# Optimization experiments

Measured on AMD Instinct MI355X. Metric: run time of the kernel, lower is better.

Reference implementation:

```python
import jax, jax.numpy as jnp
import numpy as np

D_MODEL = 1024
HEADS = 16
D_K = D_MODEL // HEADS
D_FF = 4096
EPS = 1e-6


def setup_inputs() -> dict:
    key = jax.random.key(0)
    ks = jax.random.split(key, 16)
    s = 1.0 / np.sqrt(D_MODEL)
    inp = {
        'x': jax.random.normal(ks[0], (4, 2048, D_MODEL), dtype=jnp.float32),
        'Wq': jax.random.normal(ks[1], (D_MODEL, D_MODEL), dtype=jnp.float32) * s,
        'bq': jnp.zeros((D_MODEL,), jnp.float32),
        'Wk': jax.random.normal(ks[2], (D_MODEL, D_MODEL), dtype=jnp.float32) * s,
        'bk': jnp.zeros((D_MODEL,), jnp.float32),
        'Wv': jax.random.normal(ks[3], (D_MODEL, D_MODEL), dtype=jnp.float32) * s,
        'bv': jnp.zeros((D_MODEL,), jnp.float32),
        'Wo': jax.random.normal(ks[4], (D_MODEL, D_MODEL), dtype=jnp.float32) * s,
        'bo': jnp.zeros((D_MODEL,), jnp.float32),
        'alpha1': jnp.ones((D_MODEL,), jnp.float32),
        'bias1': jnp.zeros((D_MODEL,), jnp.float32),
        'alpha2': jnp.ones((D_MODEL,), jnp.float32),
        'bias2': jnp.zeros((D_MODEL,), jnp.float32),
        'W1': jax.random.normal(ks[5], (D_MODEL, D_FF), dtype=jnp.float32) * s,
        'b1': jnp.zeros((D_FF,), jnp.float32),
        'W2': jax.random.normal(ks[6], (D_FF, D_MODEL), dtype=jnp.float32) * (1.0 / np.sqrt(D_FF)),
        'b2': jnp.zeros((D_MODEL,), jnp.float32),
    }
    return inp


def _residual_norm(x, residual, alpha, bias):
    # x = x + residual; norm with mean and UNBIASED std (torch x.std default),
    # eps added to std (not variance), affine alpha/bias. Dropout = identity (eval).
    s = x + residual
    mean = jnp.mean(s, axis=-1, keepdims=True)
    std = jnp.std(s, axis=-1, keepdims=True, ddof=1)
    return alpha * (s - mean) / (std + EPS) + bias


def _forward(x, Wq, bq, Wk, bk, Wv, bv, Wo, bo, alpha1, bias1, alpha2, bias2, W1, b1, W2, b2):
    B, S, D = x.shape
    # QKV projections and head split: (B, H, S, d_k)
    def split_heads(t):
        return t.reshape(B, S, HEADS, D_K).transpose(0, 2, 1, 3)
    Q = split_heads(x @ Wq + bq)
    K = split_heads(x @ Wk + bk)
    V = split_heads(x @ Wv + bv)
    # scaled dot-product attention (no mask, no dropout in eval)
    scores = jnp.einsum('bhqd,bhkd->bhqk', Q, K) / np.sqrt(D_K)
    weights = jax.nn.softmax(scores, axis=-1)
    attn = jnp.einsum('bhqk,bhkd->bhqd', weights, V)
    concat = attn.transpose(0, 2, 1, 3).reshape(B, S, D)
    attn_out = concat @ Wo + bo
    # post-norm residual 1
    norm1 = _residual_norm(attn_out, x, alpha1, bias1)
    # FFN (dropout = identity in eval)
    ff = jax.nn.relu(norm1 @ W1 + b1) @ W2 + b2
    # post-norm residual 2
    return _residual_norm(ff, norm1, alpha2, bias2)


def reference(x, Wq, bq, Wk, bk, Wv, bv, Wo, bo, alpha1, bias1, alpha2, bias2, W1, b1, W2, b2):
    return _forward(x, Wq, bq, Wk, bk, Wv, bv, Wo, bo, alpha1, bias1, alpha2, bias2, W1, b1, W2, b2)
```

## Files before the change

### kernel.cpp

```cpp
#include <hip/hip_runtime.h>
#include <hip/hip_bf16.h>
#include <stdint.h>

typedef __attribute__((ext_vector_type(8))) short bv8;
typedef __attribute__((ext_vector_type(4))) short sv4;
typedef __attribute__((ext_vector_type(4))) float f4;
typedef __attribute__((ext_vector_type(4))) unsigned uv4;

#define LDS_AS __attribute__((address_space(3)))
#define GLB_AS __attribute__((address_space(1)))

#if __has_builtin(__builtin_amdgcn_exp2f)
#define EXP2F(x) __builtin_amdgcn_exp2f(x)
#else
#define EXP2F(x) exp2f(x)
#endif

#define GBAR __builtin_amdgcn_s_barrier()

__device__ __forceinline__ void gload16(const void* g, void* l) {
  __builtin_amdgcn_global_load_lds((GLB_AS void*)(g), (LDS_AS void*)(l), 16, 0, 0);
}

__device__ __forceinline__ short f2bs(float x) {
  return __builtin_bit_cast(short, __float2bfloat16(x));
}
__device__ __forceinline__ float bs2f(short s) {
  unsigned u = ((unsigned)(unsigned short)s) << 16;
  return __builtin_bit_cast(float, u);
}
__device__ __forceinline__ unsigned cvtpk(float lo, float hi) {
  unsigned r;
  asm("v_cvt_pk_bf16_f32 %0, %1, %2" : "=v"(r) : "v"(lo), "v"(hi));
  return r;
}

__global__ __launch_bounds__(256) void k_prep(const float* __restrict__ x, short* __restrict__ xb,
                                              const float* __restrict__ Wq, short* __restrict__ Wqt,
                                              const float* __restrict__ Wk, short* __restrict__ Wkt,
                                              const float* __restrict__ Wv, short* __restrict__ Wvt,
                                              const float* __restrict__ Wo, short* __restrict__ Wot,
                                              const float* __restrict__ W1, short* __restrict__ W1t,
                                              const float* __restrict__ W2, short* __restrict__ W2t) {
  const int bid = blockIdx.x;
  if (bid < 8192) {
    const int i = (bid * 256 + threadIdx.x) * 4;
    const float4 v = *(const float4*)(x + i);
    sv4 o; o[0] = f2bs(v.x); o[1] = f2bs(v.y); o[2] = f2bs(v.z); o[3] = f2bs(v.w);
    *(sv4*)(xb + i) = o;
    return;
  }
  const float* W; short* Wt; int K, N, l;
  if (bid < 12288) {
    l = (bid - 8192) & 1023; K = 1024; N = 1024;
    const int sel = (bid - 8192) >> 10;
    W  = sel == 0 ? Wq  : sel == 1 ? Wk  : sel == 2 ? Wv  : Wo;
    Wt = sel == 0 ? Wqt : sel == 1 ? Wkt : sel == 2 ? Wvt : Wot;
  } else if (bid < 16384) {
    l = bid - 12288; K = 1024; N = 4096; W = W1; Wt = W1t;
  } else {
    l = bid - 16384; K = 4096; N = 1024; W = W2; Wt = W2t;
  }
  const int nb = N >> 5;
  const int n0 = (l % nb) * 32, k0 = (l / nb) * 32;
  __shared__ float tile[32][33];
  const int tx = threadIdx.x & 31, ty = threadIdx.x >> 5;
#pragma unroll
  for (int i = 0; i < 32; i += 8)
    tile[ty + i][tx] = W[(size_t)(k0 + ty + i) * N + n0 + tx];
  __syncthreads();
#pragma unroll
  for (int i = 0; i < 32; i += 8)
    Wt[(size_t)(n0 + ty + i) * K + k0 + tx] = f2bs(tile[tx][ty + i]);
}

template<int EPI, int MIH>
__global__ __launch_bounds__(512) void k_gemm8p(
    const short* __restrict__ A, const short* __restrict__ Bt,
    const float* __restrict__ bias, const float* __restrict__ bias2, const float* __restrict__ bias3,
    short* __restrict__ C, short* __restrict__ D2, short* __restrict__ D3,
    int M, int N, int K, int nbx) {
  constexpr int BM = MIH * 64;
  constexpr int HOFF = (MIH == 4) ? 16384 : 4096;
  __shared__ __align__(16) short SA[2][BM * 64];
  __shared__ __align__(16) short SB[2][256 * 64];

  const int t = threadIdx.x;
  const int lane = t & 63, w = t >> 6;
  const int wr = w >> 2, wc = w & 3;
  const int lr = lane & 15, lg = lane >> 4;
  const int cpx = gridDim.x >> 3;
  const int bid = blockIdx.x;
  const int wid = (bid & 7) * cpx + (bid >> 3);
  const int by = wid / nbx, bx = wid % nbx;
  const int m0 = by * BM, n0 = bx * 256;
  const int nt = K >> 6;
  const int swz = ((t >> 3) & 7) << 4;
  const int rbyte0 = (lg * 16) ^ ((lr & 7) << 4);
  const int rbyte1 = (64 + lg * 16) ^ ((lr & 7) << 4);

  auto ST_A = [&](int k0, int half, int buf) {
#pragma unroll
    for (int i = 0; i < 2; ++i) {
      const int L = t * 16 + i * 8192;
      const int cbs = (L & 127) ^ swz;
      const int grow = (MIH == 4) ? (m0 + i * 128 + half * 64 + (t >> 3))
                                  : (m0 + i * 64 + (t >> 3));
      gload16(A + (size_t)grow * K + k0 + (cbs >> 1),
              (char*)SA[buf] + (MIH == 4 ? half * 16384 : 0) + L);
    }
  };
  auto ST_B = [&](int k0, int half, int buf) {
#pragma unroll
    for (int i = 0; i < 2; ++i) {
      const int L = t * 16 + i * 8192;
      const int rr = (t >> 3) + i * 64;
      const int cbs = (L & 127) ^ swz;
      const int grow = n0 + (rr >> 5) * 64 + half * 32 + (rr & 31);
      gload16(Bt + (size_t)grow * K + k0 + (cbs >> 1),
              (char*)SB[buf] + half * 16384 + L);
    }
  };

  f4 acc[2 * MIH][4] = {};
  bv8 af[MIH][2], bflo[2][2], bfhi[2][2];

  auto LDA = [&](int buf, int half) {
    const char* base = (const char*)SA[buf] + half * HOFF + wr * 8192;
#pragma unroll
    for (int m = 0; m < MIH; ++m) {
      af[m][0] = *(const bv8*)(base + (m * 16 + lr) * 128 + rbyte0);
      af[m][1] = *(const bv8*)(base + (m * 16 + lr) * 128 + rbyte1);
    }
  };
  auto LDB = [&](int buf, int half, bv8 (&bf)[2][2]) {
    const char* base = (const char*)SB[buf] + half * 16384 + wc * 4096;
#pragma unroll
    for (int n = 0; n < 2; ++n) {
      bf[n][0] = *(const bv8*)(base + (n * 16 + lr) * 128 + rbyte0);
      bf[n][1] = *(const bv8*)(base + (n * 16 + lr) * 128 + rbyte1);
    }
  };
  auto MM = [&](bv8 (&bf)[2][2], int mB, int nB) {
    __builtin_amdgcn_s_setprio(1);
#pragma unroll
    for (int kk = 0; kk < 2; ++kk)
#pragma unroll
      for (int m = 0; m < MIH; ++m)
#pragma unroll
        for (int n = 0; n < 2; ++n)
          acc[mB + m][nB + n] = __builtin_amdgcn_mfma_f32_16x16x32_bf16(
              af[m][kk], bf[n][kk], acc[mB + m][nB + n], 0, 0, 0);
    __builtin_amdgcn_s_setprio(0);
  };

  ST_A(0, 0, 0); if (MIH == 4) ST_A(0, 1, 0);
  ST_B(0, 0, 0); ST_B(0, 1, 0);
  ST_A(64, 0, 1);
  ST_B(64, 1, 1);
  if (MIH == 4) { ST_A(64, 1, 1); asm volatile("s_waitcnt vmcnt(6)" ::: "memory"); }
  else          { asm volatile("s_waitcnt vmcnt(4)" ::: "memory"); }
  GBAR;

  const int nIter = nt >> 1;
  for (int it = 0; it < nIter; ++it) {
    const int k1 = (2 * it + 1) << 6;
    const int k2 = (2 * it + 2) << 6, k3 = (2 * it + 3) << 6;
    const bool h2 = (2 * it + 2) < nt, h3 = (2 * it + 3) < nt;

    LDA(0, 0); LDB(0, 0, bflo);
    ST_B(k1, 0, 1);
    GBAR; MM(bflo, 0, 0); GBAR;
    LDB(0, 1, bfhi);
    if (h2 && MIH == 4) ST_A(k2, 0, 0);
    GBAR; MM(bfhi, 0, 2); GBAR;
    LDA(0, 1);
    if (h2) ST_B(k2, 1, 0);
    GBAR; MM(bfhi, MIH, 2); GBAR;
    if (h2) ST_A(k2, (MIH == 4) ? 1 : 0, 0);
    if (h2) {
      if (MIH == 4) asm volatile("s_waitcnt vmcnt(6)" ::: "memory");
      else          asm volatile("s_waitcnt vmcnt(4)" ::: "memory");
    } else {
      asm volatile("s_waitcnt vmcnt(0)" ::: "memory");
    }
    GBAR; MM(bflo, MIH, 0); GBAR;

    LDA(1, 0); LDB(1, 0, bflo);
    if (h2) ST_B(k2, 0, 0);
    GBAR; MM(bflo, 0, 0); GBAR;
    LDB(1, 1, bfhi);
    if (h3 && MIH == 4) ST_A(k3, 0, 1);
    GBAR; MM(bfhi, 0, 2); GBAR;
    LDA(1, 1);
    if (h3) ST_B(k3, 1, 1);
    GBAR; MM(bfhi, MIH, 2); GBAR;
    if (h3) ST_A(k3, (MIH == 4) ? 1 : 0, 1);
    if (h3) {
      if (MIH == 4) asm volatile("s_waitcnt vmcnt(6)" ::: "memory");
      else          asm volatile("s_waitcnt vmcnt(4)" ::: "memory");
    } else {
      asm volatile("s_waitcnt vmcnt(0)" ::: "memory");
    }
    GBAR; MM(bflo, MIH, 0); GBAR;
  }

#pragma unroll
  for (int ni = 0; ni < 4; ++ni) {
    const int c = n0 + wc * 64 + ni * 16 + lr;
    float bvs;
    int sel = 0, h = 0, d = 0;
    if (EPI == 2) {
      sel = c >> 10; const int cc = c & 1023;
      bvs = (sel == 0 ? bias : sel == 1 ? bias2 : bias3)[cc];
      h = cc >> 6; d = cc & 63;
    } else {
      bvs = bias[c];
    }
#pragma unroll
    for (int mi = 0; mi < 2 * MIH; ++mi) {
#pragma unroll
      for (int j = 0; j < 4; ++j) {
        const int r = m0 + wr * (MIH * 32) + mi * 16 + lg * 4 + j;
        float v = acc[mi][ni][j] + bvs;
        if (EPI == 1) v = fmaxf(v, 0.f);
        if (EPI == 2) {
          const int bb = r >> 11, s = r & 2047;
          if (sel == 0)      C [((size_t)(bb * 16 + h) * 2048 + s) * 64 + d] = f2bs(v);
          else if (sel == 1) D2[((size_t)(bb * 16 + h) * 2048 + s) * 64 + d] = f2bs(v);
          else               D3[((size_t)(bb * 16 + h) * 64 + d) * 2048 + s] = f2bs(v);
        } else {
          C[(size_t)r * N + c] = f2bs(v);
        }
      }
    }
  }
}

__global__ __launch_bounds__(256) void k_attn(const short* __restrict__ Qg, const short* __restrict__ Kg,
                                              const short* __restrict__ Vtg, short* __restrict__ Oc) {
  __shared__ __align__(16) short Ks[2][128 * 64];

  const int t = threadIdx.x, lane = t & 63, w = t >> 6;
  const int lr = lane & 15, lg = lane >> 4;
  const int bid = blockIdx.x;
  const int wid = (bid & 7) * 128 + (bid >> 3);
  const int q0 = (wid & 15) * 128;
  const int bh = wid >> 4;
  const int b = bh >> 4, h = bh & 15;
  const short* Qp = Qg + (size_t)bh * 2048 * 64;
  const short* Kp = Kg + (size_t)bh * 2048 * 64;
  const short* Vp = Vtg + (size_t)bh * 64 * 2048;

  bv8 qf[2][2];
#pragma unroll
  for (int mi = 0; mi < 2; ++mi)
#pragma unroll
    for (int kk = 0; kk < 2; ++kk)
      qf[mi][kk] = *(const bv8*)(Qp + (size_t)(q0 + w * 32 + mi * 16 + lr) * 64 + kk * 32 + lg * 8);

  f4 Oa[2][4] = {};
  float lsum[2] = {0.f, 0.f};
  const float SC = 0.125f * 1.44269504089f;
  const bool hi = lg >= 2;
  const bool xx = (lg == 1) || (lg == 2);

  auto QKSM = [&](const char* Kb, int hf, bv8 (&pf)[2][2]) {
    f4 Sa[2][4] = {};
#pragma unroll
    for (int kk = 0; kk < 2; ++kk) {
      bv8 kf[4];
#pragma unroll
      for (int nl = 0; nl < 4; ++nl) {
        const int row = (hf * 4 + nl) * 16 + lr;
        const int cb = kk * 64 + lg * 16;
        kf[nl] = *(const bv8*)(Kb + row * 128 + (cb ^ ((row & 7) << 4)));
      }
      __builtin_amdgcn_s_setprio(1);
#pragma unroll
      for (int mi = 0; mi < 2; ++mi)
#pragma unroll
        for (int nl = 0; nl < 4; ++nl)
          Sa[mi][nl] = __builtin_amdgcn_mfma_f32_16x16x32_bf16(kf[nl], qf[mi][kk], Sa[mi][nl], 0, 0, 0);
      __builtin_amdgcn_s_setprio(0);
    }
#pragma unroll
    for (int mi = 0; mi < 2; ++mi) {
      float rs = 0.f;
#pragma unroll
      for (int nl = 0; nl < 4; ++nl)
#pragma unroll
        for (int j = 0; j < 4; ++j) {
          const float p = EXP2F(Sa[mi][nl][j] * SC);
          Sa[mi][nl][j] = p;
          rs += p;
        }
      lsum[mi] += rs;
    }
#pragma unroll
    for (int k2 = 0; k2 < 2; ++k2)
#pragma unroll
      for (int mi = 0; mi < 2; ++mi) {
        const unsigned W0 = cvtpk(Sa[mi][2 * k2][0], Sa[mi][2 * k2][1]);
        const unsigned W1 = cvtpk(Sa[mi][2 * k2][2], Sa[mi][2 * k2][3]);
        const unsigned W2 = cvtpk(Sa[mi][2 * k2 + 1][0], Sa[mi][2 * k2 + 1][1]);
        const unsigned W3 = cvtpk(Sa[mi][2 * k2 + 1][2], Sa[mi][2 * k2 + 1][3]);
        const unsigned w0 = hi ? W2 : W0, w1 = hi ? W3 : W1;
        const unsigned s0 = __shfl_xor(hi ? W0 : W2, 32);
        const unsigned s1 = __shfl_xor(hi ? W1 : W3, 32);
        const unsigned t0 = __shfl_xor(xx ? w0 : s0, 16);
        const unsigned t1 = __shfl_xor(xx ? w1 : s1, 16);
        uv4 u;
        u[0] = (lg == 0) ? w0 : (lg == 2) ? s0 : t0;
        u[1] = (lg == 0) ? w1 : (lg == 2) ? s1 : t1;
        u[2] = (lg == 3) ? w0 : (lg == 1) ? s0 : t0;
        u[3] = (lg == 3) ? w1 : (lg == 1) ? s1 : t1;
        pf[k2][mi] = __builtin_bit_cast(bv8, u);
      }
  };
  auto LOADV = [&](int kt, int hf, bv8 (&vf)[2][4]) {
#pragma unroll
    for (int k2 = 0; k2 < 2; ++k2)
#pragma unroll
      for (int nO = 0; nO < 4; ++nO)
        vf[k2][nO] = *(const bv8*)(Vp + (size_t)(nO * 16 + lr) * 2048 + kt + hf * 64 + k2 * 32 + lg * 8);
  };
  auto PV = [&](bv8 (&vf)[2][4], bv8 (&pf)[2][2]) {
    __builtin_amdgcn_s_setprio(1);
#pragma unroll
    for (int k2 = 0; k2 < 2; ++k2)
#pragma unroll
      for (int mi = 0; mi < 2; ++mi)
#pragma unroll
        for (int nO = 0; nO < 4; ++nO)
          Oa[mi][nO] = __builtin_amdgcn_mfma_f32_16x16x32_bf16(vf[k2][nO], pf[k2][mi], Oa[mi][nO], 0, 0, 0);
    __builtin_amdgcn_s_setprio(0);
  };

#pragma unroll
  for (int i = 0; i < 4; ++i) {
    const int L = t * 16 + i * 4096;
    const int row = L >> 7;
    const int cbs = (L & 127) ^ ((row & 7) << 4);
    gload16(Kp + (size_t)row * 64 + (cbs >> 1), (char*)Ks[0] + L);
  }
  __syncthreads();

  int cur = 0;
  for (int kt = 0; kt < 2048; kt += 128) {
    if (kt + 128 < 2048) {
#pragma unroll
      for (int i = 0; i < 4; ++i) {
        const int L = t * 16 + i * 4096;
        const int row = L >> 7;
        const int cbs = (L & 127) ^ ((row & 7) << 4);
        gload16(Kp + (size_t)(kt + 128 + row) * 64 + (cbs >> 1), (char*)Ks[cur ^ 1] + L);
      }
    }
    const char* Kb = (const char*)Ks[cur];

    bv8 vfA[2][4], vfB[2][4], pfA[2][2], pfB[2][2];
    LOADV(kt, 0, vfA);
    QKSM(Kb, 0, pfA);
    LOADV(kt, 1, vfB);
    PV(vfA, pfA);
    QKSM(Kb, 1, pfB);
    PV(vfB, pfB);

    __syncthreads();
    cur ^= 1;
  }

#pragma unroll
  for (int mi = 0; mi < 2; ++mi) {
    lsum[mi] += __shfl_xor(lsum[mi], 16);
    lsum[mi] += __shfl_xor(lsum[mi], 32);
  }

#pragma unroll
  for (int mi = 0; mi < 2; ++mi) {
    const float inv = 1.f / lsum[mi];
    const int q = q0 + w * 32 + mi * 16 + lr;
#pragma unroll
    for (int nO = 0; nO < 4; ++nO) {
      sv4 o;
#pragma unroll
      for (int j = 0; j < 4; ++j) o[j] = f2bs(Oa[mi][nO][j] * inv);
      const int c = h * 64 + nO * 16 + lg * 4;
      *(sv4*)(Oc + ((size_t)b * 2048 + q) * 1024 + c) = o;
    }
  }
}

template<int MODE>
__global__ __launch_bounds__(256) void k_resnorm(const short* __restrict__ a, const void* __restrict__ res,
                                                 const float* __restrict__ alpha, const float* __restrict__ beta,
                                                 void* __restrict__ out) {
  const int row = blockIdx.x;
  const int t = threadIdx.x;
  const int lane = t & 63, w = t >> 6;
  const size_t base = (size_t)row * 1024;

  const sv4 av = *(const sv4*)(a + base + t * 4);
  float v[4];
  if (MODE == 0) {
    const float4 rv = *(const float4*)((const float*)res + base + t * 4);
    v[0] = bs2f(av[0]) + rv.x; v[1] = bs2f(av[1]) + rv.y;
    v[2] = bs2f(av[2]) + rv.z; v[3] = bs2f(av[3]) + rv.w;
  } else {
    const sv4 rv = *(const sv4*)((const short*)res + base + t * 4);
#pragma unroll
    for (int i = 0; i < 4; ++i) v[i] = bs2f(av[i]) + bs2f(rv[i]);
  }
  float s = v[0] + v[1] + v[2] + v[3];
  float sq = v[0] * v[0] + v[1] * v[1] + v[2] * v[2] + v[3] * v[3];
#pragma unroll
  for (int m = 1; m < 64; m <<= 1) { s += __shfl_xor(s, m); sq += __shfl_xor(sq, m); }
  __shared__ float red[8];
  if (lane == 0) { red[w] = s; red[w + 4] = sq; }
  __syncthreads();
  s = red[0] + red[1] + red[2] + red[3];
  sq = red[4] + red[5] + red[6] + red[7];
  const float mean = s * (1.f / 1024.f);
  const float var = (sq - 1024.f * mean * mean) * (1.f / 1023.f);
  const float inv = 1.f / (sqrtf(fmaxf(var, 0.f)) + 1e-6f);
  const float4 al = *(const float4*)(alpha + t * 4);
  const float4 be = *(const float4*)(beta + t * 4);
  float y[4];
  y[0] = al.x * (v[0] - mean) * inv + be.x;
  y[1] = al.y * (v[1] - mean) * inv + be.y;
  y[2] = al.z * (v[2] - mean) * inv + be.z;
  y[3] = al.w * (v[3] - mean) * inv + be.w;
  if (MODE == 0) {
    sv4 o; o[0] = f2bs(y[0]); o[1] = f2bs(y[1]); o[2] = f2bs(y[2]); o[3] = f2bs(y[3]);
    *(sv4*)((short*)out + base + t * 4) = o;
  } else {
    *(float4*)((float*)out + base + t * 4) = make_float4(y[0], y[1], y[2], y[3]);
  }
}

extern "C" void kernel_launch(void* const* d_in, const int* in_sizes, int n_in,
                              void* d_out, int out_size, void* d_ws, size_t ws_size,
                              hipStream_t stream) {
  const float* x   = (const float*)d_in[0];
  const float* Wq  = (const float*)d_in[1];
  const float* bq  = (const float*)d_in[2];
  const float* Wk  = (const float*)d_in[3];
  const float* bk  = (const float*)d_in[4];
  const float* Wv  = (const float*)d_in[5];
  const float* bv  = (const float*)d_in[6];
  const float* Wo  = (const float*)d_in[7];
  const float* bo  = (const float*)d_in[8];
  const float* al1 = (const float*)d_in[9];
  const float* bi1 = (const float*)d_in[10];
  const float* al2 = (const float*)d_in[11];
  const float* bi2 = (const float*)d_in[12];
  const float* W1  = (const float*)d_in[13];
  const float* b1  = (const float*)d_in[14];
  const float* W2  = (const float*)d_in[15];
  const float* b2  = (const float*)d_in[16];

  if (ws_size < (size_t)136 * 1024 * 1024) return;

  char* ws = (char*)d_ws;
  short* xb  = (short*)(ws);
  short* Qb  = (short*)(ws + (16ll << 20));
  short* Kb  = (short*)(ws + (32ll << 20));
  short* Vtb = (short*)(ws + (48ll << 20));
  short* Hb  = (short*)(ws);
  short* Wqt = (short*)(ws + (64ll << 20));
  short* Wkt = (short*)(ws + (66ll << 20));
  short* Wvt = (short*)(ws + (68ll << 20));
  short* Wot = (short*)(ws + (70ll << 20));
  short* W1t = (short*)(ws + (72ll << 20));
  short* W2t = (short*)(ws + (80ll << 20));
  short* Cc  = (short*)(ws + (88ll << 20));
  short* AOb = (short*)(ws + (104ll << 20));
  short* N1b = (short*)(ws + (120ll << 20));
  short* FFb = (short*)(ws + (104ll << 20));

  k_prep<<<20480, 256, 0, stream>>>(x, xb, Wq, Wqt, Wk, Wkt, Wv, Wvt, Wo, Wot, W1, W1t, W2, W2t);

  k_gemm8p<2, 2><<<768, 512, 0, stream>>>(xb, Wqt, bq, bk, bv, Qb, Kb, Vtb, 8192, 3072, 1024, 12);

  k_attn<<<1024, 256, 0, stream>>>(Qb, Kb, Vtb, Cc);

  k_gemm8p<0, 2><<<256, 512, 0, stream>>>(Cc, Wot, bo, nullptr, nullptr, AOb, nullptr, nullptr,
                                          8192, 1024, 1024, 4);
  k_resnorm<0><<<8192, 256, 0, stream>>>(AOb, x, al1, bi1, N1b);

  k_gemm8p<1, 4><<<512, 512, 0, stream>>>(N1b, W1t, b1, nullptr, nullptr, Hb, nullptr, nullptr,
                                          8192, 4096, 1024, 16);
  k_gemm8p<0, 2><<<256, 512, 0, stream>>>(Hb, W2t, b2, nullptr, nullptr, FFb, nullptr, nullptr,
                                          8192, 1024, 4096, 4);
  k_resnorm<1><<<8192, 256, 0, stream>>>(FFb, N1b, al2, bi2, (float*)d_out);
}
```

Before: 449.7 us.

## Stage transposed V epilogue through LDS and prefetch V fragments ahead

The QKV GEMM epilogue for the V section now writes bias-added bf16 results into a shared LDS buffer in transposed layout, then emits coalesced 16-byte row stores to the V^T output. The previous path did scattered 2-byte strided stores. The attention kernel also software-pipelines the V fragment loads by issuing the first half-tile load for the next iteration early. The LDS transpose path only writes output when MIH==2, so other tile configurations would silently skip V output. The prefetch adds register pressure.

```diff
diff --git a/kernel.cpp b/kernel.cpp
--- a/kernel.cpp
+++ b/kernel.cpp
@@ -82,8 +82,8 @@
     int M, int N, int K, int nbx) {
   constexpr int BM = MIH * 64;
   constexpr int HOFF = (MIH == 4) ? 16384 : 4096;
-  __shared__ __align__(16) short SA[2][BM * 64];
-  __shared__ __align__(16) short SB[2][256 * 64];
+  constexpr int SBOFF = 2 * BM * 128;
+  __shared__ __align__(16) char LDSBUF[SBOFF + 65536];
 
   const int t = threadIdx.x;
   const int lane = t & 63, w = t >> 6;
@@ -99,6 +99,9 @@
   const int rbyte0 = (lg * 16) ^ ((lr & 7) << 4);
   const int rbyte1 = (64 + lg * 16) ^ ((lr & 7) << 4);
 
+  auto SAb = [&](int buf) -> char* { return LDSBUF + buf * (BM * 128); };
+  auto SBb = [&](int buf) -> char* { return LDSBUF + SBOFF + buf * 32768; };
+
   auto ST_A = [&](int k0, int half, int buf) {
 #pragma unroll
     for (int i = 0; i < 2; ++i) {
@@ -107,7 +110,7 @@
       const int grow = (MIH == 4) ? (m0 + i * 128 + half * 64 + (t >> 3))
                                   : (m0 + i * 64 + (t >> 3));
       gload16(A + (size_t)grow * K + k0 + (cbs >> 1),
-              (char*)SA[buf] + (MIH == 4 ? half * 16384 : 0) + L);
+              SAb(buf) + (MIH == 4 ? half * 16384 : 0) + L);
     }
   };
   auto ST_B = [&](int k0, int half, int buf) {
@@ -118,7 +121,7 @@
       const int cbs = (L & 127) ^ swz;
       const int grow = n0 + (rr >> 5) * 64 + half * 32 + (rr & 31);
       gload16(Bt + (size_t)grow * K + k0 + (cbs >> 1),
-              (char*)SB[buf] + half * 16384 + L);
+              SBb(buf) + half * 16384 + L);
     }
   };
 
@@ -126,7 +129,7 @@
   bv8 af[MIH][2], bflo[2][2], bfhi[2][2];
 
   auto LDA = [&](int buf, int half) {
-    const char* base = (const char*)SA[buf] + half * HOFF + wr * 8192;
+    const char* base = SAb(buf) + half * HOFF + wr * 8192;
 #pragma unroll
     for (int m = 0; m < MIH; ++m) {
       af[m][0] = *(const bv8*)(base + (m * 16 + lr) * 128 + rbyte0);
@@ -134,7 +137,7 @@
     }
   };
   auto LDB = [&](int buf, int half, bv8 (&bf)[2][2]) {
-    const char* base = (const char*)SB[buf] + half * 16384 + wc * 4096;
+    const char* base = SBb(buf) + half * 16384 + wc * 4096;
 #pragma unroll
     for (int n = 0; n < 2; ++n) {
       bf[n][0] = *(const bv8*)(base + (n * 16 + lr) * 128 + rbyte0);
@@ -205,6 +208,36 @@
     GBAR; MM(bflo, MIH, 0); GBAR;
   }
 
+  if (EPI == 2 && (n0 >> 10) == 2) {
+    short* TR = (short*)LDSBUF;
+    __syncthreads();
+#pragma unroll
+    for (int ni = 0; ni < 4; ++ni) {
+      const int dloc = wc * 64 + ni * 16 + lr;
+      const float bvs = bias3[(n0 - 2048) + dloc];
+#pragma unroll
+      for (int mi = 0; mi < 2 * MIH; ++mi) {
+        const int sloc = wr * (MIH * 32) + mi * 16 + lg * 4;
+        sv4 pk;
+#pragma unroll
+        for (int j = 0; j < 4; ++j) pk[j] = f2bs(acc[mi][ni][j] + bvs);
+        *(sv4*)(TR + dloc * 136 + sloc) = pk;
+      }
+    }
+    __syncthreads();
+    const int bb = m0 >> 11, s0r = m0 & 2047;
+    const int dd = t >> 1, sh = (t & 1) * 64;
+    const int dg = (n0 - 2048) + dd;
+    const int hh = dg >> 6, dl = dg & 63;
+    short* dst = D3 + ((size_t)(bb * 16 + hh) * 64 + dl) * 2048 + s0r + sh;
+    if (MIH == 2) {
+#pragma unroll
+      for (int i = 0; i < 8; ++i)
+        *(bv8*)(dst + i * 8) = *(const bv8*)(TR + dd * 136 + sh + i * 8);
+    }
+    return;
+  }
+
 #pragma unroll
   for (int ni = 0; ni < 4; ++ni) {
     const int c = n0 + wc * 64 + ni * 16 + lr;
@@ -212,7 +245,7 @@
     int sel = 0, h = 0, d = 0;
     if (EPI == 2) {
       sel = c >> 10; const int cc = c & 1023;
-      bvs = (sel == 0 ? bias : sel == 1 ? bias2 : bias3)[cc];
+      bvs = (sel == 0 ? bias : bias2)[cc];
       h = cc >> 6; d = cc & 63;
     } else {
       bvs = bias[c];
@@ -226,9 +259,8 @@
         if (EPI == 1) v = fmaxf(v, 0.f);
         if (EPI == 2) {
           const int bb = r >> 11, s = r & 2047;
-          if (sel == 0)      C [((size_t)(bb * 16 + h) * 2048 + s) * 64 + d] = f2bs(v);
-          else if (sel == 1) D2[((size_t)(bb * 16 + h) * 2048 + s) * 64 + d] = f2bs(v);
-          else               D3[((size_t)(bb * 16 + h) * 64 + d) * 2048 + s] = f2bs(v);
+          if (sel == 0) C [((size_t)(bb * 16 + h) * 2048 + s) * 64 + d] = f2bs(v);
+          else          D2[((size_t)(bb * 16 + h) * 2048 + s) * 64 + d] = f2bs(v);
         } else {
           C[(size_t)r * N + c] = f2bs(v);
         }
@@ -344,6 +376,8 @@
     const int cbs = (L & 127) ^ ((row & 7) << 4);
     gload16(Kp + (size_t)row * 64 + (cbs >> 1), (char*)Ks[0] + L);
   }
+  bv8 vfA[2][4], vfB[2][4];
+  LOADV(0, 0, vfA);
   __syncthreads();
 
   int cur = 0;
@@ -359,12 +393,12 @@
     }
     const char* Kb = (const char*)Ks[cur];
 
-    bv8 vfA[2][4], vfB[2][4], pfA[2][2], pfB[2][2];
-    LOADV(kt, 0, vfA);
+    bv8 pfA[2][2], pfB[2][2];
     QKSM(Kb, 0, pfA);
     LOADV(kt, 1, vfB);
     PV(vfA, pfA);
     QKSM(Kb, 1, pfB);
+    if (kt + 128 < 2048) LOADV(kt + 128, 0, vfA);
     PV(vfB, pfB);
 
     __syncthreads();
```

Result: slower. 519.2 us (+15.4%).
